# Kernel tuning notes

Measured on AMD Instinct MI355X. Metric: run time of the kernel, lower is better.

## Reference

```python
import jax, jax.numpy as jnp
import numpy as np

N_NODES = 50000
N_EDGES = 300000
DIM = 256
ALPHA = 0.1  # residual mixing with initial features, as passed in forward


def gcn_layer(x0, x, edge_idx, W):
    """One GraphConvolution call: mean neighbor aggregation over the edge
    list, GCNII-style residual mix with initial features x0, then linear."""
    src, dst = edge_idx[0], edge_idx[1]
    msgs = x[src]  # [E, D] gather
    agg = jax.ops.segment_sum(msgs, dst, num_segments=x.shape[0])
    deg = jax.ops.segment_sum(jnp.ones((src.shape[0],), x.dtype), dst,
                              num_segments=x.shape[0])
    agg = agg / jnp.maximum(deg, 1.0)[:, None]
    h = ALPHA * x0 + (1.0 - ALPHA) * agg
    return h @ W


def setup_inputs() -> dict:
    key = jax.random.key(0)
    k1, k2, k3 = jax.random.split(key, 3)
    x = jax.random.normal(k1, (N_NODES, DIM), dtype=jnp.float32)
    edge_idx = jax.random.randint(k2, (2, N_EDGES), 0, N_NODES, dtype=jnp.int64)
    W = jax.random.normal(k3, (DIM, DIM), dtype=jnp.float32) / np.sqrt(DIM)
    return {"drug_cell_pair_feature": x, "edge_idx": edge_idx, "W": W}


def reference(drug_cell_pair_feature, edge_idx, W):
    x0 = drug_cell_pair_feature
    out = jax.nn.relu(gcn_layer(x0, x0, edge_idx, W))
    for _ in range(4):  # 4 more identical calls, always mixing with x0
        out = jax.nn.relu(gcn_layer(x0, out, edge_idx, W))
    return out
```

## Files before the change

### kernel.cpp

```cpp
#include <hip/hip_runtime.h>

#define DIM 256
#define SCAN_B 256

typedef __attribute__((ext_vector_type(8))) short short8;
typedef __attribute__((ext_vector_type(8))) unsigned short u16x8;
typedef __attribute__((ext_vector_type(4))) float f32x4;

__device__ __forceinline__ unsigned short f32_to_bf16(float x) {
    unsigned int u = __float_as_uint(x);
    unsigned int r = u + 0x7FFFu + ((u >> 16) & 1u);
    return (unsigned short)(r >> 16);
}
__device__ __forceinline__ float bf16_to_f32(unsigned short h) {
    return __uint_as_float(((unsigned int)h) << 16);
}

__device__ __forceinline__ void load_lds16(const void* g, void* l) {
    __builtin_amdgcn_global_load_lds(
        (const __attribute__((address_space(1))) unsigned int*)g,
        (__attribute__((address_space(3))) unsigned int*)l, 16, 0, 0);
}

__global__ void deg_kernel(const int* __restrict__ dst, int E, int* __restrict__ deg) {
    int e = blockIdx.x * blockDim.x + threadIdx.x;
    if (e < E) atomicAdd(&deg[dst[e]], 1);
}

__global__ void scan1_kernel(const int* __restrict__ deg, int N,
                             int* __restrict__ excl, int* __restrict__ bsums) {
    __shared__ int s[SCAN_B];
    int tid = threadIdx.x;
    int i = blockIdx.x * SCAN_B + tid;
    int v = (i < N) ? deg[i] : 0;
    s[tid] = v;
    __syncthreads();
    #pragma unroll
    for (int off = 1; off < SCAN_B; off <<= 1) {
        int t = (tid >= off) ? s[tid - off] : 0;
        __syncthreads();
        s[tid] += t;
        __syncthreads();
    }
    if (i <= N) excl[i] = s[tid] - v;
    if (tid == SCAN_B - 1) bsums[blockIdx.x] = s[tid];
}

__global__ void scan2_kernel(int* __restrict__ bsums, int nb) {
    __shared__ int s[SCAN_B];
    int tid = threadIdx.x;
    int v = (tid < nb) ? bsums[tid] : 0;
    s[tid] = v;
    __syncthreads();
    #pragma unroll
    for (int off = 1; off < SCAN_B; off <<= 1) {
        int t = (tid >= off) ? s[tid - off] : 0;
        __syncthreads();
        s[tid] += t;
        __syncthreads();
    }
    if (tid < nb) bsums[tid] = s[tid] - v;
}

__global__ void scan3_kernel(const int* __restrict__ excl, const int* __restrict__ bsums,
                             const int* __restrict__ deg, int N,
                             int* __restrict__ row_start, float* __restrict__ inv_deg) {
    int i = blockIdx.x * SCAN_B + threadIdx.x;
    if (i <= N) row_start[i] = excl[i] + bsums[blockIdx.x];
    if (i < N) inv_deg[i] = 1.0f / (float)max(deg[i], 1);
}

__global__ void fill_kernel(const int* __restrict__ src, const int* __restrict__ dst, int E,
                            const int* __restrict__ row_start, int* __restrict__ cursor,
                            int* __restrict__ csr_src) {
    int e = blockIdx.x * blockDim.x + threadIdx.x;
    if (e < E) {
        int d = dst[e];
        int pos = row_start[d] + atomicAdd(&cursor[d], 1);
        csr_src[pos] = src[e];
    }
}

__global__ void prep_kernel(const float* __restrict__ W, unsigned short* __restrict__ Wt,
                            const float* __restrict__ x0, unsigned short* __restrict__ x0b,
                            int n4) {
    int b = blockIdx.x;
    if (b < DIM) {
        int k = b, n = threadIdx.x;
        Wt[n * DIM + k] = f32_to_bf16(W[k * DIM + n]);
    } else {
        int i = (b - DIM) * 256 + threadIdx.x;
        if (i < n4) {
            float4 v = ((const float4*)x0)[i];
            ushort4 o;
            o.x = f32_to_bf16(v.x); o.y = f32_to_bf16(v.y);
            o.z = f32_to_bf16(v.z); o.w = f32_to_bf16(v.w);
            ((ushort4*)x0b)[i] = o;
        }
    }
}

__global__ __launch_bounds__(256) void aggregate_kernel(
    const unsigned short* __restrict__ xh, const unsigned short* __restrict__ x0b,
    const int* __restrict__ row_start, const int* __restrict__ csr_src,
    const float* __restrict__ inv_deg,
    unsigned short* __restrict__ h, int N)
{
    int node = blockIdx.x * 4 + (threadIdx.x >> 6);
    if (node >= N) return;
    const int lane = threadIdx.x & 63;
    const int half = lane >> 5;
    const int c    = (lane & 31) * 8;

    int beg = row_start[node];
    int end = row_start[node + 1];

    float a[8];
    #pragma unroll
    for (int j = 0; j < 8; j++) a[j] = 0.f;

    int e = beg;
    for (; e + 4 <= end; e += 4) {
        int s0 = csr_src[e + half];
        int s1 = csr_src[e + 2 + half];
        u16x8 v0 = *(const u16x8*)(xh + (size_t)s0 * DIM + c);
        u16x8 v1 = *(const u16x8*)(xh + (size_t)s1 * DIM + c);
        #pragma unroll
        for (int j = 0; j < 8; j++) a[j] += bf16_to_f32(v0[j]) + bf16_to_f32(v1[j]);
    }
    if (e + 2 <= end) {
        int s0 = csr_src[e + half];
        u16x8 v0 = *(const u16x8*)(xh + (size_t)s0 * DIM + c);
        #pragma unroll
        for (int j = 0; j < 8; j++) a[j] += bf16_to_f32(v0[j]);
        e += 2;
    }
    if (e < end && half == 0) {
        int s0 = csr_src[e];
        u16x8 v0 = *(const u16x8*)(xh + (size_t)s0 * DIM + c);
        #pragma unroll
        for (int j = 0; j < 8; j++) a[j] += bf16_to_f32(v0[j]);
    }

    #pragma unroll
    for (int j = 0; j < 8; j++) a[j] += __shfl_xor(a[j], 32);

    if (half == 0) {
        float scale = 0.9f * inv_deg[node];
        u16x8 xv = *(const u16x8*)(x0b + (size_t)node * DIM + c);
        u16x8 o;
        #pragma unroll
        for (int j = 0; j < 8; j++)
            o[j] = f32_to_bf16(0.1f * bf16_to_f32(xv[j]) + scale * a[j]);
        *(u16x8*)(h + (size_t)node * DIM + c) = o;
    }
}

template <bool LAST>
__global__ __launch_bounds__(256) void gemm_kernel(
    const unsigned short* __restrict__ h, const unsigned short* __restrict__ Wt,
    float* __restrict__ out_f32, unsigned short* __restrict__ out_bf16, int N)
{
    __shared__ unsigned short As[128 * 32];
    __shared__ unsigned short Bs[128 * 32];

    const int t    = threadIdx.x;
    const int w    = t >> 6;
    const int lane = t & 63;
    const int lm   = lane & 15;
    const int q    = lane >> 4;
    const int wm   = w >> 1, wn = w & 1;
    const int m0   = blockIdx.x * 128;
    const int n0   = blockIdx.y * 128;

    const int sr = t >> 2;
    const int sg = (t & 3) * 8;

    f32x4 acc[4][4];
    #pragma unroll
    for (int mi = 0; mi < 4; mi++)
        #pragma unroll
        for (int ni = 0; ni < 4; ni++)
            acc[mi][ni] = (f32x4){0.f, 0.f, 0.f, 0.f};

    for (int kb = 0; kb < DIM; kb += 32) {
        __syncthreads();
        #pragma unroll
        for (int half = 0; half < 2; half++) {
            int r = half * 64 + sr;
            int ldso = (half * 256 + t) * 8;
            load_lds16(h  + (size_t)(m0 + r) * DIM + kb + sg, &As[ldso]);
            load_lds16(Wt + (size_t)(n0 + r) * DIM + kb + sg, &Bs[ldso]);
        }
        __syncthreads();

        short8 a[4];
        #pragma unroll
        for (int mi = 0; mi < 4; mi++) {
            int row = wm * 64 + mi * 16 + lm;
            a[mi] = *(const short8*)&As[row * 32 + q * 8];
        }
        #pragma unroll
        for (int ni = 0; ni < 4; ni++) {
            int row = wn * 64 + ni * 16 + lm;
            short8 b = *(const short8*)&Bs[row * 32 + q * 8];
            #pragma unroll
            for (int mi = 0; mi < 4; mi++)
                acc[mi][ni] = __builtin_amdgcn_mfma_f32_16x16x32_bf16(a[mi], b, acc[mi][ni], 0, 0, 0);
        }
    }

    #pragma unroll
    for (int mi = 0; mi < 4; mi++) {
        const int rowb = m0 + wm * 64 + mi * 16 + q * 4;
        #pragma unroll
        for (int ni = 0; ni < 4; ni++) {
            const int col = n0 + wn * 64 + ni * 16 + lm;
            #pragma unroll
            for (int r = 0; r < 4; r++) {
                int row = rowb + r;
                if (row < N) {
                    float v = fmaxf(acc[mi][ni][r], 0.0f);
                    if (LAST) out_f32[(size_t)row * DIM + col] = v;
                    else      out_bf16[(size_t)row * DIM + col] = f32_to_bf16(v);
                }
            }
        }
    }
}

extern "C" void kernel_launch(void* const* d_in, const int* in_sizes, int n_in,
                              void* d_out, int out_size, void* d_ws, size_t ws_size,
                              hipStream_t stream) {
    const float* x0  = (const float*)d_in[0];
    const int*   ei  = (const int*)d_in[1];
    const float* W   = (const float*)d_in[2];
    float*       out = (float*)d_out;

    const int N = in_sizes[0] / DIM;
    const int E = in_sizes[1] / 2;
    const int N_pad = (N + 127) & ~127;
    const int* src = ei;
    const int* dst = ei + E;

    const int nb = (N + 1 + SCAN_B - 1) / SCAN_B;

    char* ws = (char*)d_ws;
    size_t off = 0;
    auto alloc = [&](size_t bytes) { char* p = ws + off; off += (bytes + 15) & ~size_t(15); return p; };
    unsigned short* h       = (unsigned short*)alloc((size_t)N_pad * DIM * 2);
    unsigned short* act     = (unsigned short*)alloc((size_t)N_pad * DIM * 2);
    unsigned short* x0b     = (unsigned short*)alloc((size_t)N_pad * DIM * 2);
    unsigned short* Wt      = (unsigned short*)alloc((size_t)DIM * DIM * 2);
    float* inv_deg  = (float*)alloc((size_t)N * 4);
    int*   deg      = (int*)  alloc((size_t)N * 4 * 2);
    int*   cursor   = deg + N;
    int*   row_start= (int*)  alloc((size_t)(N + 1) * 4);
    int*   excl     = (int*)  alloc((size_t)(N + 1) * 4);
    int*   bsums    = (int*)  alloc((size_t)nb * 4);
    int*   csr_src  = (int*)  alloc((size_t)E * 4);

    hipMemsetAsync(deg, 0, (size_t)N * 4 * 2, stream);
    deg_kernel<<<(E + 255) / 256, 256, 0, stream>>>(dst, E, deg);
    scan1_kernel<<<nb, SCAN_B, 0, stream>>>(deg, N, excl, bsums);
    scan2_kernel<<<1, SCAN_B, 0, stream>>>(bsums, nb);
    scan3_kernel<<<nb, SCAN_B, 0, stream>>>(excl, bsums, deg, N, row_start, inv_deg);
    fill_kernel<<<(E + 255) / 256, 256, 0, stream>>>(src, dst, E, row_start, cursor, csr_src);
    const int n4 = N * DIM / 4;
    prep_kernel<<<DIM + (n4 + 255) / 256, 256, 0, stream>>>(W, Wt, x0, x0b, n4);

    dim3 ggrid(N_pad / 128, 2);
    for (int layer = 0; layer < 5; layer++) {
        const unsigned short* gsrc = (layer == 0) ? x0b : act;
        aggregate_kernel<<<(N + 3) / 4, 256, 0, stream>>>(gsrc, x0b, row_start, csr_src,
                                                          inv_deg, h, N);
        if (layer == 4)
            gemm_kernel<true><<<ggrid, 256, 0, stream>>>(h, Wt, out, nullptr, N);
        else
            gemm_kernel<false><<<ggrid, 256, 0, stream>>>(h, Wt, nullptr, act, N);
    }
}
```

Before: 384.3 us.

## Fuse neighbor aggregation and GEMM into one per-layer kernel

Merges the aggregate and GEMM kernels so each block aggregates 64 nodes straight into LDS as bf16, then multiplies by W with MFMA, reading W fragments directly from global memory. This drops the round trip of the intermediate h matrix through HBM and halves the kernel launches per layer. The cost is that each block now computes all 256 output columns, the aggregation loop is serialized over 16 rows per wave, and W is read per block without LDS staging, which may lower overlap between gather and compute.

```diff
diff --git a/kernel.cpp b/kernel.cpp
--- a/kernel.cpp
+++ b/kernel.cpp
@@ -14,12 +14,6 @@
 }
 __device__ __forceinline__ float bf16_to_f32(unsigned short h) {
     return __uint_as_float(((unsigned int)h) << 16);
-}
-
-__device__ __forceinline__ void load_lds16(const void* g, void* l) {
-    __builtin_amdgcn_global_load_lds(
-        (const __attribute__((address_space(1))) unsigned int*)g,
-        (__attribute__((address_space(3))) unsigned int*)l, 16, 0, 0);
 }
 
 __global__ void deg_kernel(const int* __restrict__ dst, int E, int* __restrict__ deg) {
@@ -100,81 +94,75 @@
     }
 }
 
-__global__ __launch_bounds__(256) void aggregate_kernel(
-    const unsigned short* __restrict__ xh, const unsigned short* __restrict__ x0b,
+template <bool LAST>
+__global__ __launch_bounds__(256) void layer_kernel(
+    const unsigned short* __restrict__ act_in, const unsigned short* __restrict__ x0b,
     const int* __restrict__ row_start, const int* __restrict__ csr_src,
-    const float* __restrict__ inv_deg,
-    unsigned short* __restrict__ h, int N)
-{
-    int node = blockIdx.x * 4 + (threadIdx.x >> 6);
-    if (node >= N) return;
-    const int lane = threadIdx.x & 63;
-    const int half = lane >> 5;
-    const int c    = (lane & 31) * 8;
-
-    int beg = row_start[node];
-    int end = row_start[node + 1];
-
-    float a[8];
-    #pragma unroll
-    for (int j = 0; j < 8; j++) a[j] = 0.f;
-
-    int e = beg;
-    for (; e + 4 <= end; e += 4) {
-        int s0 = csr_src[e + half];
-        int s1 = csr_src[e + 2 + half];
-        u16x8 v0 = *(const u16x8*)(xh + (size_t)s0 * DIM + c);
-        u16x8 v1 = *(const u16x8*)(xh + (size_t)s1 * DIM + c);
-        #pragma unroll
-        for (int j = 0; j < 8; j++) a[j] += bf16_to_f32(v0[j]) + bf16_to_f32(v1[j]);
-    }
-    if (e + 2 <= end) {
-        int s0 = csr_src[e + half];
-        u16x8 v0 = *(const u16x8*)(xh + (size_t)s0 * DIM + c);
-        #pragma unroll
-        for (int j = 0; j < 8; j++) a[j] += bf16_to_f32(v0[j]);
-        e += 2;
-    }
-    if (e < end && half == 0) {
-        int s0 = csr_src[e];
-        u16x8 v0 = *(const u16x8*)(xh + (size_t)s0 * DIM + c);
-        #pragma unroll
-        for (int j = 0; j < 8; j++) a[j] += bf16_to_f32(v0[j]);
-    }
-
-    #pragma unroll
-    for (int j = 0; j < 8; j++) a[j] += __shfl_xor(a[j], 32);
-
-    if (half == 0) {
-        float scale = 0.9f * inv_deg[node];
-        u16x8 xv = *(const u16x8*)(x0b + (size_t)node * DIM + c);
-        u16x8 o;
-        #pragma unroll
-        for (int j = 0; j < 8; j++)
-            o[j] = f32_to_bf16(0.1f * bf16_to_f32(xv[j]) + scale * a[j]);
-        *(u16x8*)(h + (size_t)node * DIM + c) = o;
-    }
-}
-
-template <bool LAST>
-__global__ __launch_bounds__(256) void gemm_kernel(
-    const unsigned short* __restrict__ h, const unsigned short* __restrict__ Wt,
+    const float* __restrict__ inv_deg, const unsigned short* __restrict__ Wt,
     float* __restrict__ out_f32, unsigned short* __restrict__ out_bf16, int N)
 {
-    __shared__ unsigned short As[128 * 32];
-    __shared__ unsigned short Bs[128 * 32];
+    __shared__ unsigned short As[8 * 64 * 32];
 
     const int t    = threadIdx.x;
     const int w    = t >> 6;
     const int lane = t & 63;
     const int lm   = lane & 15;
     const int q    = lane >> 4;
-    const int wm   = w >> 1, wn = w & 1;
-    const int m0   = blockIdx.x * 128;
-    const int n0   = blockIdx.y * 128;
-
-    const int sr = t >> 2;
-    const int sg = (t & 3) * 8;
+    const int m0   = blockIdx.x * 64;
+    const int half = lane >> 5;
+    const int c    = (lane & 31) * 8;
+    const int ckb  = c >> 5;
+    const int cko  = c & 31;
+
+    #pragma unroll 1
+    for (int i = 0; i < 16; i++) {
+        int r = i * 4 + w;
+        int node = m0 + r;
+        if (node >= N) continue;
+        int beg = row_start[node];
+        int end = row_start[node + 1];
+
+        float a[8];
+        #pragma unroll
+        for (int j = 0; j < 8; j++) a[j] = 0.f;
+
+        int e = beg;
+        for (; e + 4 <= end; e += 4) {
+            int s0 = csr_src[e + half];
+            int s1 = csr_src[e + 2 + half];
+            u16x8 v0 = *(const u16x8*)(act_in + (size_t)s0 * DIM + c);
+            u16x8 v1 = *(const u16x8*)(act_in + (size_t)s1 * DIM + c);
+            #pragma unroll
+            for (int j = 0; j < 8; j++) a[j] += bf16_to_f32(v0[j]) + bf16_to_f32(v1[j]);
+        }
+        if (e + 2 <= end) {
+            int s0 = csr_src[e + half];
+            u16x8 v0 = *(const u16x8*)(act_in + (size_t)s0 * DIM + c);
+            #pragma unroll
+            for (int j = 0; j < 8; j++) a[j] += bf16_to_f32(v0[j]);
+            e += 2;
+        }
+        if (e < end && half == 0) {
+            int s0 = csr_src[e];
+            u16x8 v0 = *(const u16x8*)(act_in + (size_t)s0 * DIM + c);
+            #pragma unroll
+            for (int j = 0; j < 8; j++) a[j] += bf16_to_f32(v0[j]);
+        }
+
+        #pragma unroll
+        for (int j = 0; j < 8; j++) a[j] += __shfl_xor(a[j], 32);
+
+        if (half == 0) {
+            float scale = 0.9f * inv_deg[node];
+            u16x8 xv = *(const u16x8*)(x0b + (size_t)node * DIM + c);
+            u16x8 o;
+            #pragma unroll
+            for (int j = 0; j < 8; j++)
+                o[j] = f32_to_bf16(0.1f * bf16_to_f32(xv[j]) + scale * a[j]);
+            *(u16x8*)&As[ckb * 2048 + r * 32 + cko] = o;
+        }
+    }
+    __syncthreads();
 
     f32x4 acc[4][4];
     #pragma unroll
@@ -183,44 +171,37 @@
         for (int ni = 0; ni < 4; ni++)
             acc[mi][ni] = (f32x4){0.f, 0.f, 0.f, 0.f};
 
-    for (int kb = 0; kb < DIM; kb += 32) {
-        __syncthreads();
-        #pragma unroll
-        for (int half = 0; half < 2; half++) {
-            int r = half * 64 + sr;
-            int ldso = (half * 256 + t) * 8;
-            load_lds16(h  + (size_t)(m0 + r) * DIM + kb + sg, &As[ldso]);
-            load_lds16(Wt + (size_t)(n0 + r) * DIM + kb + sg, &Bs[ldso]);
-        }
-        __syncthreads();
-
+    #pragma unroll 1
+    for (int kb = 0; kb < 8; kb++) {
+        short8 b[4];
+        #pragma unroll
+        for (int ni = 0; ni < 4; ni++) {
+            int n = w * 64 + ni * 16 + lm;
+            b[ni] = *(const short8*)(Wt + (size_t)n * DIM + kb * 32 + q * 8);
+        }
         short8 a[4];
         #pragma unroll
-        for (int mi = 0; mi < 4; mi++) {
-            int row = wm * 64 + mi * 16 + lm;
-            a[mi] = *(const short8*)&As[row * 32 + q * 8];
-        }
+        for (int mi = 0; mi < 4; mi++)
+            a[mi] = *(const short8*)&As[kb * 2048 + (mi * 16 + lm) * 32 + q * 8];
         #pragma unroll
         for (int ni = 0; ni < 4; ni++) {
-            int row = wn * 64 + ni * 16 + lm;
-            short8 b = *(const short8*)&Bs[row * 32 + q * 8];
             #pragma unroll
             for (int mi = 0; mi < 4; mi++)
-                acc[mi][ni] = __builtin_amdgcn_mfma_f32_16x16x32_bf16(a[mi], b, acc[mi][ni], 0, 0, 0);
+                acc[mi][ni] = __builtin_amdgcn_mfma_f32_16x16x32_bf16(a[mi], b[ni], acc[mi][ni], 0, 0, 0);
         }
     }
 
     #pragma unroll
     for (int mi = 0; mi < 4; mi++) {
-        const int rowb = m0 + wm * 64 + mi * 16 + q * 4;
+        const int rowb = m0 + mi * 16 + q * 4;
         #pragma unroll
         for (int ni = 0; ni < 4; ni++) {
-            const int col = n0 + wn * 64 + ni * 16 + lm;
-            #pragma unroll
-            for (int r = 0; r < 4; r++) {
-                int row = rowb + r;
+            const int col = w * 64 + ni * 16 + lm;
+            #pragma unroll
+            for (int r4 = 0; r4 < 4; r4++) {
+                int row = rowb + r4;
                 if (row < N) {
-                    float v = fmaxf(acc[mi][ni][r], 0.0f);
+                    float v = fmaxf(acc[mi][ni][r4], 0.0f);
                     if (LAST) out_f32[(size_t)row * DIM + col] = v;
                     else      out_bf16[(size_t)row * DIM + col] = f32_to_bf16(v);
                 }
@@ -239,7 +220,7 @@
 
     const int N = in_sizes[0] / DIM;
     const int E = in_sizes[1] / 2;
-    const int N_pad = (N + 127) & ~127;
+    const int N_pad = (N + 63) & ~63;
     const int* src = ei;
     const int* dst = ei + E;
 
@@ -248,8 +229,8 @@
     char* ws = (char*)d_ws;
     size_t off = 0;
     auto alloc = [&](size_t bytes) { char* p = ws + off; off += (bytes + 15) & ~size_t(15); return p; };
-    unsigned short* h       = (unsigned short*)alloc((size_t)N_pad * DIM * 2);
-    unsigned short* act     = (unsigned short*)alloc((size_t)N_pad * DIM * 2);
+    unsigned short* act_a   = (unsigned short*)alloc((size_t)N_pad * DIM * 2);
+    unsigned short* act_b   = (unsigned short*)alloc((size_t)N_pad * DIM * 2);
     unsigned short* x0b     = (unsigned short*)alloc((size_t)N_pad * DIM * 2);
     unsigned short* Wt      = (unsigned short*)alloc((size_t)DIM * DIM * 2);
     float* inv_deg  = (float*)alloc((size_t)N * 4);
@@ -269,14 +250,10 @@
     const int n4 = N * DIM / 4;
     prep_kernel<<<DIM + (n4 + 255) / 256, 256, 0, stream>>>(W, Wt, x0, x0b, n4);
 
-    dim3 ggrid(N_pad / 128, 2);
-    for (int layer = 0; layer < 5; layer++) {
-        const unsigned short* gsrc = (layer == 0) ? x0b : act;
-        aggregate_kernel<<<(N + 3) / 4, 256, 0, stream>>>(gsrc, x0b, row_start, csr_src,
-                                                          inv_deg, h, N);
-        if (layer == 4)
-            gemm_kernel<true><<<ggrid, 256, 0, stream>>>(h, Wt, out, nullptr, N);
-        else
-            gemm_kernel<false><<<ggrid, 256, 0, stream>>>(h, Wt, nullptr, act, N);
-    }
-}
+    const int grid = N_pad / 64;
+    layer_kernel<false><<<grid, 256, 0, stream>>>(x0b,   x0b, row_start, csr_src, inv_deg, Wt, nullptr, act_a, N);
+    layer_kernel<false><<<grid, 256, 0, stream>>>(act_a, x0b, row_start, csr_src, inv_deg, Wt, nullptr, act_b, N);
+    layer_kernel<false><<<grid, 256, 0, stream>>>(act_b, x0b, row_start, csr_src, inv_deg, Wt, nullptr, act_a, N);
+    layer_kernel<false><<<grid, 256, 0, stream>>>(act_a, x0b, row_start, csr_src, inv_deg, Wt, nullptr, act_b, N);
+    layer_kernel<true ><<<grid, 256, 0, stream>>>(act_b, x0b, row_start, csr_src, inv_deg, Wt, out, nullptr, N);
+}
```

After: 576.8 us. 50.1% more time.

## Fuse all stages into one persistent kernel with hierarchical grid barriers

Applied to the files above, without the earlier changes.

Replaces the chain of separate launches (degree count, three-pass scan, CSR fill, prep, and five aggregate plus GEMM pairs) with a single persistent kernel of 1280 blocks. Stages are separated by a software grid barrier that uses per-subgroup atomic counters and a top-level counter. The goal is to remove the launch overhead and tail gaps between the roughly 17 small kernels. In exchange it depends on all blocks being co-resident (launch bounds of 5 blocks per CU) to avoid deadlock, may lose occupancy and the compiler's restrict/const optimisations, and alternates two activation buffers.

```diff
diff --git a/kernel.cpp b/kernel.cpp
--- a/kernel.cpp
+++ b/kernel.cpp
@@ -1,7 +1,9 @@
 #include <hip/hip_runtime.h>
 
 #define DIM 256
-#define SCAN_B 256
+#define G 1280
+#define NSUB 16
+#define SUBSZ (G / NSUB)
 
 typedef __attribute__((ext_vector_type(8))) short short8;
 typedef __attribute__((ext_vector_type(8))) unsigned short u16x8;
@@ -22,210 +24,224 @@
         (__attribute__((address_space(3))) unsigned int*)l, 16, 0, 0);
 }
 
-__global__ void deg_kernel(const int* __restrict__ dst, int E, int* __restrict__ deg) {
-    int e = blockIdx.x * blockDim.x + threadIdx.x;
-    if (e < E) atomicAdd(&deg[dst[e]], 1);
-}
-
-__global__ void scan1_kernel(const int* __restrict__ deg, int N,
-                             int* __restrict__ excl, int* __restrict__ bsums) {
-    __shared__ int s[SCAN_B];
-    int tid = threadIdx.x;
-    int i = blockIdx.x * SCAN_B + tid;
-    int v = (i < N) ? deg[i] : 0;
-    s[tid] = v;
+__device__ __forceinline__ void gsync(int* bar, int round) {
     __syncthreads();
-    #pragma unroll
-    for (int off = 1; off < SCAN_B; off <<= 1) {
-        int t = (tid >= off) ? s[tid - off] : 0;
-        __syncthreads();
-        s[tid] += t;
-        __syncthreads();
-    }
-    if (i <= N) excl[i] = s[tid] - v;
-    if (tid == SCAN_B - 1) bsums[blockIdx.x] = s[tid];
-}
-
-__global__ void scan2_kernel(int* __restrict__ bsums, int nb) {
-    __shared__ int s[SCAN_B];
-    int tid = threadIdx.x;
-    int v = (tid < nb) ? bsums[tid] : 0;
-    s[tid] = v;
+    if (threadIdx.x == 0) {
+        __threadfence();
+        int sub = blockIdx.x & (NSUB - 1);
+        int prev = atomicAdd(&bar[sub * 32], 1);
+        if (prev == round * SUBSZ + (SUBSZ - 1))
+            atomicAdd(&bar[NSUB * 32], 1);
+        while (__hip_atomic_load(&bar[NSUB * 32], __ATOMIC_RELAXED,
+                                 __HIP_MEMORY_SCOPE_AGENT) < (round + 1) * NSUB)
+            __builtin_amdgcn_s_sleep(1);
+        __threadfence();
+    }
     __syncthreads();
-    #pragma unroll
-    for (int off = 1; off < SCAN_B; off <<= 1) {
-        int t = (tid >= off) ? s[tid - off] : 0;
-        __syncthreads();
-        s[tid] += t;
-        __syncthreads();
-    }
-    if (tid < nb) bsums[tid] = s[tid] - v;
-}
-
-__global__ void scan3_kernel(const int* __restrict__ excl, const int* __restrict__ bsums,
-                             const int* __restrict__ deg, int N,
-                             int* __restrict__ row_start, float* __restrict__ inv_deg) {
-    int i = blockIdx.x * SCAN_B + threadIdx.x;
-    if (i <= N) row_start[i] = excl[i] + bsums[blockIdx.x];
-    if (i < N) inv_deg[i] = 1.0f / (float)max(deg[i], 1);
-}
-
-__global__ void fill_kernel(const int* __restrict__ src, const int* __restrict__ dst, int E,
-                            const int* __restrict__ row_start, int* __restrict__ cursor,
-                            int* __restrict__ csr_src) {
-    int e = blockIdx.x * blockDim.x + threadIdx.x;
-    if (e < E) {
-        int d = dst[e];
+}
+
+__global__ __launch_bounds__(256, 5) void mega_kernel(
+    const float* x0, const int* eidx, const float* W,
+    int N, int E, int nb, int ntiles, int ngroups, int n4,
+    int* deg, int* row_start, int* excl, int* bsums, float* inv_deg,
+    int* csr_src, unsigned short* Wt, unsigned short* x0b,
+    unsigned short* h, unsigned short* act_a, unsigned short* act_b,
+    float* out, int* bar)
+{
+    const int* srcp = eidx;
+    const int* dstp = eidx + E;
+    int* cursor = deg + N;
+
+    __shared__ unsigned short As[128 * 32];
+    __shared__ unsigned short Bs[128 * 32];
+
+    const int tid = threadIdx.x;
+    const int bid = blockIdx.x;
+    const int gthread = bid * 256 + tid;
+    const int GT = G * 256;
+    int round = 0;
+
+    for (int i = gthread; i < 2 * N; i += GT) deg[i] = 0;
+    gsync(bar, round++);
+
+    for (int e = gthread; e < E; e += GT) atomicAdd(&deg[dstp[e]], 1);
+    gsync(bar, round++);
+
+    {
+        int* s = (int*)As;
+        if (bid < nb) {
+            int i = bid * 256 + tid;
+            int v = (i < N) ? deg[i] : 0;
+            s[tid] = v;
+            __syncthreads();
+            for (int off = 1; off < 256; off <<= 1) {
+                int t2 = (tid >= off) ? s[tid - off] : 0;
+                __syncthreads();
+                s[tid] += t2;
+                __syncthreads();
+            }
+            if (i <= N) excl[i] = s[tid] - v;
+            if (tid == 255) bsums[bid] = s[tid];
+        }
+    }
+    gsync(bar, round++);
+
+    {
+        int* s = (int*)As;
+        if (bid == 0) {
+            int v = (tid < nb) ? bsums[tid] : 0;
+            s[tid] = v;
+            __syncthreads();
+            for (int off = 1; off < 256; off <<= 1) {
+                int t2 = (tid >= off) ? s[tid - off] : 0;
+                __syncthreads();
+                s[tid] += t2;
+                __syncthreads();
+            }
+            if (tid < nb) bsums[tid] = s[tid] - v;
+        }
+    }
+    gsync(bar, round++);
+
+    if (bid < nb) {
+        int i = bid * 256 + tid;
+        if (i <= N) row_start[i] = excl[i] + bsums[bid];
+        if (i < N) inv_deg[i] = 1.0f / (float)max(deg[i], 1);
+    }
+    gsync(bar, round++);
+
+    for (int e = gthread; e < E; e += GT) {
+        int d = dstp[e];
         int pos = row_start[d] + atomicAdd(&cursor[d], 1);
-        csr_src[pos] = src[e];
-    }
-}
-
-__global__ void prep_kernel(const float* __restrict__ W, unsigned short* __restrict__ Wt,
-                            const float* __restrict__ x0, unsigned short* __restrict__ x0b,
-                            int n4) {
-    int b = blockIdx.x;
-    if (b < DIM) {
-        int k = b, n = threadIdx.x;
-        Wt[n * DIM + k] = f32_to_bf16(W[k * DIM + n]);
-    } else {
-        int i = (b - DIM) * 256 + threadIdx.x;
-        if (i < n4) {
-            float4 v = ((const float4*)x0)[i];
-            ushort4 o;
-            o.x = f32_to_bf16(v.x); o.y = f32_to_bf16(v.y);
-            o.z = f32_to_bf16(v.z); o.w = f32_to_bf16(v.w);
-            ((ushort4*)x0b)[i] = o;
-        }
-    }
-}
-
-__global__ __launch_bounds__(256) void aggregate_kernel(
-    const unsigned short* __restrict__ xh, const unsigned short* __restrict__ x0b,
-    const int* __restrict__ row_start, const int* __restrict__ csr_src,
-    const float* __restrict__ inv_deg,
-    unsigned short* __restrict__ h, int N)
-{
-    int node = blockIdx.x * 4 + (threadIdx.x >> 6);
-    if (node >= N) return;
-    const int lane = threadIdx.x & 63;
+        csr_src[pos] = srcp[e];
+    }
+    if (bid < DIM) Wt[tid * DIM + bid] = f32_to_bf16(W[bid * DIM + tid]);
+    for (int i = gthread; i < n4; i += GT) {
+        float4 v = ((const float4*)x0)[i];
+        ushort4 o;
+        o.x = f32_to_bf16(v.x); o.y = f32_to_bf16(v.y);
+        o.z = f32_to_bf16(v.z); o.w = f32_to_bf16(v.w);
+        ((ushort4*)x0b)[i] = o;
+    }
+    gsync(bar, round++);
+
+    const int w    = tid >> 6;
+    const int lane = tid & 63;
     const int half = lane >> 5;
     const int c    = (lane & 31) * 8;
-
-    int beg = row_start[node];
-    int end = row_start[node + 1];
-
-    float a[8];
-    #pragma unroll
-    for (int j = 0; j < 8; j++) a[j] = 0.f;
-
-    int e = beg;
-    for (; e + 4 <= end; e += 4) {
-        int s0 = csr_src[e + half];
-        int s1 = csr_src[e + 2 + half];
-        u16x8 v0 = *(const u16x8*)(xh + (size_t)s0 * DIM + c);
-        u16x8 v1 = *(const u16x8*)(xh + (size_t)s1 * DIM + c);
-        #pragma unroll
-        for (int j = 0; j < 8; j++) a[j] += bf16_to_f32(v0[j]) + bf16_to_f32(v1[j]);
-    }
-    if (e + 2 <= end) {
-        int s0 = csr_src[e + half];
-        u16x8 v0 = *(const u16x8*)(xh + (size_t)s0 * DIM + c);
-        #pragma unroll
-        for (int j = 0; j < 8; j++) a[j] += bf16_to_f32(v0[j]);
-        e += 2;
-    }
-    if (e < end && half == 0) {
-        int s0 = csr_src[e];
-        u16x8 v0 = *(const u16x8*)(xh + (size_t)s0 * DIM + c);
-        #pragma unroll
-        for (int j = 0; j < 8; j++) a[j] += bf16_to_f32(v0[j]);
-    }
-
-    #pragma unroll
-    for (int j = 0; j < 8; j++) a[j] += __shfl_xor(a[j], 32);
-
-    if (half == 0) {
-        float scale = 0.9f * inv_deg[node];
-        u16x8 xv = *(const u16x8*)(x0b + (size_t)node * DIM + c);
-        u16x8 o;
-        #pragma unroll
-        for (int j = 0; j < 8; j++)
-            o[j] = f32_to_bf16(0.1f * bf16_to_f32(xv[j]) + scale * a[j]);
-        *(u16x8*)(h + (size_t)node * DIM + c) = o;
-    }
-}
-
-template <bool LAST>
-__global__ __launch_bounds__(256) void gemm_kernel(
-    const unsigned short* __restrict__ h, const unsigned short* __restrict__ Wt,
-    float* __restrict__ out_f32, unsigned short* __restrict__ out_bf16, int N)
-{
-    __shared__ unsigned short As[128 * 32];
-    __shared__ unsigned short Bs[128 * 32];
-
-    const int t    = threadIdx.x;
-    const int w    = t >> 6;
-    const int lane = t & 63;
     const int lm   = lane & 15;
     const int q    = lane >> 4;
-    const int wm   = w >> 1, wn = w & 1;
-    const int m0   = blockIdx.x * 128;
-    const int n0   = blockIdx.y * 128;
-
-    const int sr = t >> 2;
-    const int sg = (t & 3) * 8;
-
-    f32x4 acc[4][4];
-    #pragma unroll
-    for (int mi = 0; mi < 4; mi++)
-        #pragma unroll
-        for (int ni = 0; ni < 4; ni++)
-            acc[mi][ni] = (f32x4){0.f, 0.f, 0.f, 0.f};
-
-    for (int kb = 0; kb < DIM; kb += 32) {
-        __syncthreads();
-        #pragma unroll
-        for (int half = 0; half < 2; half++) {
-            int r = half * 64 + sr;
-            int ldso = (half * 256 + t) * 8;
-            load_lds16(h  + (size_t)(m0 + r) * DIM + kb + sg, &As[ldso]);
-            load_lds16(Wt + (size_t)(n0 + r) * DIM + kb + sg, &Bs[ldso]);
-        }
-        __syncthreads();
-
-        short8 a[4];
-        #pragma unroll
-        for (int mi = 0; mi < 4; mi++) {
-            int row = wm * 64 + mi * 16 + lm;
-            a[mi] = *(const short8*)&As[row * 32 + q * 8];
-        }
-        #pragma unroll
-        for (int ni = 0; ni < 4; ni++) {
-            int row = wn * 64 + ni * 16 + lm;
-            short8 b = *(const short8*)&Bs[row * 32 + q * 8];
+    const int sr   = tid >> 2;
+    const int sg   = (tid & 3) * 8;
+
+    const unsigned short* gsrc = x0b;
+    for (int L = 0; L < 5; L++) {
+        for (int vg = bid; vg < ngroups; vg += G) {
+            int node = vg * 4 + w;
+            if (node < N) {
+                int beg = row_start[node];
+                int end = row_start[node + 1];
+                float a[8];
+                #pragma unroll
+                for (int j = 0; j < 8; j++) a[j] = 0.f;
+                int e = beg;
+                for (; e + 4 <= end; e += 4) {
+                    int s0 = csr_src[e + half];
+                    int s1 = csr_src[e + 2 + half];
+                    u16x8 v0 = *(const u16x8*)(gsrc + (size_t)s0 * DIM + c);
+                    u16x8 v1 = *(const u16x8*)(gsrc + (size_t)s1 * DIM + c);
+                    #pragma unroll
+                    for (int j = 0; j < 8; j++) a[j] += bf16_to_f32(v0[j]) + bf16_to_f32(v1[j]);
+                }
+                if (e + 2 <= end) {
+                    int s0 = csr_src[e + half];
+                    u16x8 v0 = *(const u16x8*)(gsrc + (size_t)s0 * DIM + c);
+                    #pragma unroll
+                    for (int j = 0; j < 8; j++) a[j] += bf16_to_f32(v0[j]);
+                    e += 2;
+                }
+                if (e < end && half == 0) {
+                    int s0 = csr_src[e];
+                    u16x8 v0 = *(const u16x8*)(gsrc + (size_t)s0 * DIM + c);
+                    #pragma unroll
+                    for (int j = 0; j < 8; j++) a[j] += bf16_to_f32(v0[j]);
+                }
+                #pragma unroll
+                for (int j = 0; j < 8; j++) a[j] += __shfl_xor(a[j], 32);
+                if (half == 0) {
+                    float scale = 0.9f * inv_deg[node];
+                    u16x8 xv = *(const u16x8*)(x0b + (size_t)node * DIM + c);
+                    u16x8 o;
+                    #pragma unroll
+                    for (int j = 0; j < 8; j++)
+                        o[j] = f32_to_bf16(0.1f * bf16_to_f32(xv[j]) + scale * a[j]);
+                    *(u16x8*)(h + (size_t)node * DIM + c) = o;
+                }
+            }
+        }
+        gsync(bar, round++);
+
+        unsigned short* actout = (L & 1) ? act_b : act_a;
+        const bool lastL = (L == 4);
+        for (int vt = bid; vt < ntiles; vt += G) {
+            const int m0 = (vt >> 1) * 128;
+            const int n0 = (vt & 1) * 128;
+            const int wm = w >> 1, wn = w & 1;
+
+            f32x4 acc[4][4];
             #pragma unroll
             for (int mi = 0; mi < 4; mi++)
-                acc[mi][ni] = __builtin_amdgcn_mfma_f32_16x16x32_bf16(a[mi], b, acc[mi][ni], 0, 0, 0);
-        }
-    }
-
-    #pragma unroll
-    for (int mi = 0; mi < 4; mi++) {
-        const int rowb = m0 + wm * 64 + mi * 16 + q * 4;
-        #pragma unroll
-        for (int ni = 0; ni < 4; ni++) {
-            const int col = n0 + wn * 64 + ni * 16 + lm;
+                #pragma unroll
+                for (int ni = 0; ni < 4; ni++)
+                    acc[mi][ni] = (f32x4){0.f, 0.f, 0.f, 0.f};
+
+            for (int kb = 0; kb < DIM; kb += 32) {
+                __syncthreads();
+                #pragma unroll
+                for (int hf = 0; hf < 2; hf++) {
+                    int r = hf * 64 + sr;
+                    int ldso = (hf * 256 + tid) * 8;
+                    load_lds16(h  + (size_t)(m0 + r) * DIM + kb + sg, &As[ldso]);
+                    load_lds16(Wt + (size_t)(n0 + r) * DIM + kb + sg, &Bs[ldso]);
+                }
+                __syncthreads();
+
+                short8 a[4];
+                #pragma unroll
+                for (int mi = 0; mi < 4; mi++) {
+                    int row = wm * 64 + mi * 16 + lm;
+                    a[mi] = *(const short8*)&As[row * 32 + q * 8];
+                }
+                #pragma unroll
+                for (int ni = 0; ni < 4; ni++) {
+                    int row = wn * 64 + ni * 16 + lm;
+                    short8 b = *(const short8*)&Bs[row * 32 + q * 8];
+                    #pragma unroll
+                    for (int mi = 0; mi < 4; mi++)
+                        acc[mi][ni] = __builtin_amdgcn_mfma_f32_16x16x32_bf16(a[mi], b, acc[mi][ni], 0, 0, 0);
+                }
+            }
+
             #pragma unroll
-            for (int r = 0; r < 4; r++) {
-                int row = rowb + r;
-                if (row < N) {
-                    float v = fmaxf(acc[mi][ni][r], 0.0f);
-                    if (LAST) out_f32[(size_t)row * DIM + col] = v;
-                    else      out_bf16[(size_t)row * DIM + col] = f32_to_bf16(v);
-                }
-            }
-        }
+            for (int mi = 0; mi < 4; mi++) {
+                const int rowb = m0 + wm * 64 + mi * 16 + q * 4;
+                #pragma unroll
+                for (int ni = 0; ni < 4; ni++) {
+                    const int col = n0 + wn * 64 + ni * 16 + lm;
+                    #pragma unroll
+                    for (int r4 = 0; r4 < 4; r4++) {
+                        int row = rowb + r4;
+                        if (row < N) {
+                            float v = fmaxf(acc[mi][ni][r4], 0.0f);
+                            if (lastL) out[(size_t)row * DIM + col] = v;
+                            else       actout[(size_t)row * DIM + col] = f32_to_bf16(v);
+                        }
+                    }
+                }
+            }
+        }
+        if (L < 4) gsync(bar, round++);
+        gsrc = actout;
     }
 }
 
@@ -240,43 +256,30 @@
     const int N = in_sizes[0] / DIM;
     const int E = in_sizes[1] / 2;
     const int N_pad = (N + 127) & ~127;
-    const int* src = ei;
-    const int* dst = ei + E;
-
-    const int nb = (N + 1 + SCAN_B - 1) / SCAN_B;
+
+    const int nb      = (N + 1 + 255) / 256;
+    const int ntiles  = (N_pad / 128) * 2;
+    const int ngroups = (N + 3) / 4;
+    const int n4      = N * DIM / 4;
 
     char* ws = (char*)d_ws;
     size_t off = 0;
-    auto alloc = [&](size_t bytes) { char* p = ws + off; off += (bytes + 15) & ~size_t(15); return p; };
+    auto alloc = [&](size_t bytes) { char* p = ws + off; off += (bytes + 255) & ~size_t(255); return p; };
     unsigned short* h       = (unsigned short*)alloc((size_t)N_pad * DIM * 2);
-    unsigned short* act     = (unsigned short*)alloc((size_t)N_pad * DIM * 2);
+    unsigned short* act_a   = (unsigned short*)alloc((size_t)N_pad * DIM * 2);
+    unsigned short* act_b   = (unsigned short*)alloc((size_t)N_pad * DIM * 2);
     unsigned short* x0b     = (unsigned short*)alloc((size_t)N_pad * DIM * 2);
     unsigned short* Wt      = (unsigned short*)alloc((size_t)DIM * DIM * 2);
     float* inv_deg  = (float*)alloc((size_t)N * 4);
     int*   deg      = (int*)  alloc((size_t)N * 4 * 2);
-    int*   cursor   = deg + N;
     int*   row_start= (int*)  alloc((size_t)(N + 1) * 4);
     int*   excl     = (int*)  alloc((size_t)(N + 1) * 4);
     int*   bsums    = (int*)  alloc((size_t)nb * 4);
     int*   csr_src  = (int*)  alloc((size_t)E * 4);
-
-    hipMemsetAsync(deg, 0, (size_t)N * 4 * 2, stream);
-    deg_kernel<<<(E + 255) / 256, 256, 0, stream>>>(dst, E, deg);
-    scan1_kernel<<<nb, SCAN_B, 0, stream>>>(deg, N, excl, bsums);
-    scan2_kernel<<<1, SCAN_B, 0, stream>>>(bsums, nb);
-    scan3_kernel<<<nb, SCAN_B, 0, stream>>>(excl, bsums, deg, N, row_start, inv_deg);
-    fill_kernel<<<(E + 255) / 256, 256, 0, stream>>>(src, dst, E, row_start, cursor, csr_src);
-    const int n4 = N * DIM / 4;
-    prep_kernel<<<DIM + (n4 + 255) / 256, 256, 0, stream>>>(W, Wt, x0, x0b, n4);
-
-    dim3 ggrid(N_pad / 128, 2);
-    for (int layer = 0; layer < 5; layer++) {
-        const unsigned short* gsrc = (layer == 0) ? x0b : act;
-        aggregate_kernel<<<(N + 3) / 4, 256, 0, stream>>>(gsrc, x0b, row_start, csr_src,
-                                                          inv_deg, h, N);
-        if (layer == 4)
-            gemm_kernel<true><<<ggrid, 256, 0, stream>>>(h, Wt, out, nullptr, N);
-        else
-            gemm_kernel<false><<<ggrid, 256, 0, stream>>>(h, Wt, nullptr, act, N);
-    }
-}
+    int*   bar      = (int*)  alloc((size_t)(NSUB * 32 + 32) * 4);
+
+    hipMemsetAsync(bar, 0, (size_t)(NSUB * 32 + 32) * 4, stream);
+    mega_kernel<<<G, 256, 0, stream>>>(x0, ei, W, N, E, nb, ntiles, ngroups, n4,
+                                       deg, row_start, excl, bsums, inv_deg,
+                                       csr_src, Wt, x0b, h, act_a, act_b, out, bar);
+}
```

Measured after the change: 1.320 ms. 3.43x slower.

## Merge CSR preprocessing kernels and retile GEMM to full-width 64x256 blocks

Applied to the files above, without the earlier changes.

Fuses the degree atomic count with the weight transpose and x0 bf16 conversion into one launch. It also replaces the three-pass block scan with a single-block chunked scan that writes row_start, cursor and inv_deg, so fill no longer adds row_start. The GEMM now uses 64-row tiles covering all 256 output columns, so each A row is loaded once. The trade-offs are a serial single-block scan with strided reads and more B traffic per block.

```diff
diff --git a/kernel.cpp b/kernel.cpp
--- a/kernel.cpp
+++ b/kernel.cpp
@@ -1,7 +1,7 @@
 #include <hip/hip_runtime.h>
 
 #define DIM 256
-#define SCAN_B 256
+#define SCAN_T 1024
 
 typedef __attribute__((ext_vector_type(8))) short short8;
 typedef __attribute__((ext_vector_type(8))) unsigned short u16x8;
@@ -22,74 +22,20 @@
         (__attribute__((address_space(3))) unsigned int*)l, 16, 0, 0);
 }
 
-__global__ void deg_kernel(const int* __restrict__ dst, int E, int* __restrict__ deg) {
-    int e = blockIdx.x * blockDim.x + threadIdx.x;
-    if (e < E) atomicAdd(&deg[dst[e]], 1);
-}
-
-__global__ void scan1_kernel(const int* __restrict__ deg, int N,
-                             int* __restrict__ excl, int* __restrict__ bsums) {
-    __shared__ int s[SCAN_B];
-    int tid = threadIdx.x;
-    int i = blockIdx.x * SCAN_B + tid;
-    int v = (i < N) ? deg[i] : 0;
-    s[tid] = v;
-    __syncthreads();
-    #pragma unroll
-    for (int off = 1; off < SCAN_B; off <<= 1) {
-        int t = (tid >= off) ? s[tid - off] : 0;
-        __syncthreads();
-        s[tid] += t;
-        __syncthreads();
-    }
-    if (i <= N) excl[i] = s[tid] - v;
-    if (tid == SCAN_B - 1) bsums[blockIdx.x] = s[tid];
-}
-
-__global__ void scan2_kernel(int* __restrict__ bsums, int nb) {
-    __shared__ int s[SCAN_B];
-    int tid = threadIdx.x;
-    int v = (tid < nb) ? bsums[tid] : 0;
-    s[tid] = v;
-    __syncthreads();
-    #pragma unroll
-    for (int off = 1; off < SCAN_B; off <<= 1) {
-        int t = (tid >= off) ? s[tid - off] : 0;
-        __syncthreads();
-        s[tid] += t;
-        __syncthreads();
-    }
-    if (tid < nb) bsums[tid] = s[tid] - v;
-}
-
-__global__ void scan3_kernel(const int* __restrict__ excl, const int* __restrict__ bsums,
-                             const int* __restrict__ deg, int N,
-                             int* __restrict__ row_start, float* __restrict__ inv_deg) {
-    int i = blockIdx.x * SCAN_B + threadIdx.x;
-    if (i <= N) row_start[i] = excl[i] + bsums[blockIdx.x];
-    if (i < N) inv_deg[i] = 1.0f / (float)max(deg[i], 1);
-}
-
-__global__ void fill_kernel(const int* __restrict__ src, const int* __restrict__ dst, int E,
-                            const int* __restrict__ row_start, int* __restrict__ cursor,
-                            int* __restrict__ csr_src) {
-    int e = blockIdx.x * blockDim.x + threadIdx.x;
-    if (e < E) {
-        int d = dst[e];
-        int pos = row_start[d] + atomicAdd(&cursor[d], 1);
-        csr_src[pos] = src[e];
-    }
-}
-
-__global__ void prep_kernel(const float* __restrict__ W, unsigned short* __restrict__ Wt,
-                            const float* __restrict__ x0, unsigned short* __restrict__ x0b,
-                            int n4) {
-    int b = blockIdx.x;
-    if (b < DIM) {
-        int k = b, n = threadIdx.x;
-        Wt[n * DIM + k] = f32_to_bf16(W[k * DIM + n]);
+__global__ void degprep_kernel(const int* __restrict__ dst, int E, int* __restrict__ deg,
+                               const float* __restrict__ W, unsigned short* __restrict__ Wt,
+                               const float* __restrict__ x0, unsigned short* __restrict__ x0b,
+                               int n4, int nd) {
+    const int b = blockIdx.x;
+    const int tid = threadIdx.x;
+    if (b < nd) {
+        int e = b * 256 + tid;
+        if (e < E) atomicAdd(&deg[dst[e]], 1);
+    } else if (b < nd + DIM) {
+        int k = b - nd;
+        Wt[tid * DIM + k] = f32_to_bf16(W[k * DIM + tid]);
     } else {
-        int i = (b - DIM) * 256 + threadIdx.x;
+        int i = (b - nd - DIM) * 256 + tid;
         if (i < n4) {
             float4 v = ((const float4*)x0)[i];
             ushort4 o;
@@ -97,6 +43,52 @@
             o.z = f32_to_bf16(v.z); o.w = f32_to_bf16(v.w);
             ((ushort4*)x0b)[i] = o;
         }
+    }
+}
+
+__global__ __launch_bounds__(SCAN_T) void scan_kernel(
+    const int* __restrict__ deg, int N,
+    int* __restrict__ row_start, int* __restrict__ cursor, float* __restrict__ inv_deg)
+{
+    __shared__ int tsum[SCAN_T];
+    const int tid = threadIdx.x;
+    const int ch = (N + SCAN_T) / SCAN_T;
+    const int base = tid * ch;
+
+    int s = 0;
+    for (int i = 0; i < ch; i++) {
+        int idx = base + i;
+        if (idx < N) s += deg[idx];
+    }
+    tsum[tid] = s;
+    __syncthreads();
+    for (int off = 1; off < SCAN_T; off <<= 1) {
+        int v = (tid >= off) ? tsum[tid - off] : 0;
+        __syncthreads();
+        tsum[tid] += v;
+        __syncthreads();
+    }
+    int run = (tid > 0) ? tsum[tid - 1] : 0;
+    for (int i = 0; i < ch; i++) {
+        int idx = base + i;
+        if (idx <= N) {
+            row_start[idx] = run;
+            if (idx < N) {
+                int d = deg[idx];
+                cursor[idx] = run;
+                inv_deg[idx] = 1.0f / (float)max(d, 1);
+                run += d;
+            }
+        }
+    }
+}
+
+__global__ void fill_kernel(const int* __restrict__ src, const int* __restrict__ dst, int E,
+                            int* __restrict__ cursor, int* __restrict__ csr_src) {
+    int e = blockIdx.x * blockDim.x + threadIdx.x;
+    if (e < E) {
+        int pos = atomicAdd(&cursor[dst[e]], 1);
+        csr_src[pos] = src[e];
     }
 }
 
@@ -161,20 +153,17 @@
     const unsigned short* __restrict__ h, const unsigned short* __restrict__ Wt,
     float* __restrict__ out_f32, unsigned short* __restrict__ out_bf16, int N)
 {
-    __shared__ unsigned short As[128 * 32];
-    __shared__ unsigned short Bs[128 * 32];
+    __shared__ unsigned short As[64 * 32];
+    __shared__ unsigned short Bs[256 * 32];
 
     const int t    = threadIdx.x;
     const int w    = t >> 6;
     const int lane = t & 63;
     const int lm   = lane & 15;
     const int q    = lane >> 4;
-    const int wm   = w >> 1, wn = w & 1;
-    const int m0   = blockIdx.x * 128;
-    const int n0   = blockIdx.y * 128;
-
-    const int sr = t >> 2;
-    const int sg = (t & 3) * 8;
+    const int m0   = blockIdx.x * 64;
+    const int sr   = t >> 2;
+    const int sg   = (t & 3) * 8;
 
     f32x4 acc[4][4];
     #pragma unroll
@@ -185,25 +174,19 @@
 
     for (int kb = 0; kb < DIM; kb += 32) {
         __syncthreads();
-        #pragma unroll
-        for (int half = 0; half < 2; half++) {
-            int r = half * 64 + sr;
-            int ldso = (half * 256 + t) * 8;
-            load_lds16(h  + (size_t)(m0 + r) * DIM + kb + sg, &As[ldso]);
-            load_lds16(Wt + (size_t)(n0 + r) * DIM + kb + sg, &Bs[ldso]);
-        }
+        load_lds16(h + (size_t)(m0 + sr) * DIM + kb + sg, &As[t * 8]);
+        #pragma unroll
+        for (int hf = 0; hf < 4; hf++)
+            load_lds16(Wt + (size_t)(hf * 64 + sr) * DIM + kb + sg, &Bs[hf * 2048 + t * 8]);
         __syncthreads();
 
         short8 a[4];
         #pragma unroll
-        for (int mi = 0; mi < 4; mi++) {
-            int row = wm * 64 + mi * 16 + lm;
-            a[mi] = *(const short8*)&As[row * 32 + q * 8];
-        }
+        for (int mi = 0; mi < 4; mi++)
+            a[mi] = *(const short8*)&As[(mi * 16 + lm) * 32 + q * 8];
         #pragma unroll
         for (int ni = 0; ni < 4; ni++) {
-            int row = wn * 64 + ni * 16 + lm;
-            short8 b = *(const short8*)&Bs[row * 32 + q * 8];
+            short8 b = *(const short8*)&Bs[(w * 64 + ni * 16 + lm) * 32 + q * 8];
             #pragma unroll
             for (int mi = 0; mi < 4; mi++)
                 acc[mi][ni] = __builtin_amdgcn_mfma_f32_16x16x32_bf16(a[mi], b, acc[mi][ni], 0, 0, 0);
@@ -212,10 +195,10 @@
 
     #pragma unroll
     for (int mi = 0; mi < 4; mi++) {
-        const int rowb = m0 + wm * 64 + mi * 16 + q * 4;
+        const int rowb = m0 + mi * 16 + q * 4;
         #pragma unroll
         for (int ni = 0; ni < 4; ni++) {
-            const int col = n0 + wn * 64 + ni * 16 + lm;
+            const int col = w * 64 + ni * 16 + lm;
             #pragma unroll
             for (int r = 0; r < 4; r++) {
                 int row = rowb + r;
@@ -243,7 +226,9 @@
     const int* src = ei;
     const int* dst = ei + E;
 
-    const int nb = (N + 1 + SCAN_B - 1) / SCAN_B;
+    const int nd = (E + 255) / 256;
+    const int n4 = N * DIM / 4;
+    const int np = (n4 + 255) / 256;
 
     char* ws = (char*)d_ws;
     size_t off = 0;
@@ -253,23 +238,17 @@
     unsigned short* x0b     = (unsigned short*)alloc((size_t)N_pad * DIM * 2);
     unsigned short* Wt      = (unsigned short*)alloc((size_t)DIM * DIM * 2);
     float* inv_deg  = (float*)alloc((size_t)N * 4);
-    int*   deg      = (int*)  alloc((size_t)N * 4 * 2);
-    int*   cursor   = deg + N;
+    int*   deg      = (int*)  alloc((size_t)N * 4);
+    int*   cursor   = (int*)  alloc((size_t)N * 4);
     int*   row_start= (int*)  alloc((size_t)(N + 1) * 4);
-    int*   excl     = (int*)  alloc((size_t)(N + 1) * 4);
-    int*   bsums    = (int*)  alloc((size_t)nb * 4);
     int*   csr_src  = (int*)  alloc((size_t)E * 4);
 
-    hipMemsetAsync(deg, 0, (size_t)N * 4 * 2, stream);
-    deg_kernel<<<(E + 255) / 256, 256, 0, stream>>>(dst, E, deg);
-    scan1_kernel<<<nb, SCAN_B, 0, stream>>>(deg, N, excl, bsums);
-    scan2_kernel<<<1, SCAN_B, 0, stream>>>(bsums, nb);
-    scan3_kernel<<<nb, SCAN_B, 0, stream>>>(excl, bsums, deg, N, row_start, inv_deg);
-    fill_kernel<<<(E + 255) / 256, 256, 0, stream>>>(src, dst, E, row_start, cursor, csr_src);
-    const int n4 = N * DIM / 4;
-    prep_kernel<<<DIM + (n4 + 255) / 256, 256, 0, stream>>>(W, Wt, x0, x0b, n4);
-
-    dim3 ggrid(N_pad / 128, 2);
+    hipMemsetAsync(deg, 0, (size_t)N * 4, stream);
+    degprep_kernel<<<nd + DIM + np, 256, 0, stream>>>(dst, E, deg, W, Wt, x0, x0b, n4, nd);
+    scan_kernel<<<1, SCAN_T, 0, stream>>>(deg, N, row_start, cursor, inv_deg);
+    fill_kernel<<<nd, 256, 0, stream>>>(src, dst, E, cursor, csr_src);
+
+    const int ggrid = N_pad / 64;
     for (int layer = 0; layer < 5; layer++) {
         const unsigned short* gsrc = (layer == 0) ? x0b : act;
         aggregate_kernel<<<(N + 3) / 4, 256, 0, stream>>>(gsrc, x0b, row_start, csr_src,
```

New measurement: 519.8 us. +35.2%, slower.
